# Kernel tuning notes

Measured on AMD Instinct MI355X. Metric: run time of the kernel, lower is better.

## Reference

```python
import jax, jax.numpy as jnp
import numpy as np

D_K = 64

def setup_inputs() -> dict:
    key = jax.random.key(0)
    k1, k2, k3, k4 = jax.random.split(key, 4)
    B, H, S = 2, 16, 2048
    Q = jax.random.normal(k1, (B, H, S, D_K), dtype=jnp.float32)
    K = jax.random.normal(k2, (B, H, S, D_K), dtype=jnp.float32)
    V = jax.random.normal(k3, (B, H, S, D_K), dtype=jnp.float32)
    attn_mask = jax.random.randint(k4, (B, H, S, S), 0, 2) == 1
    return {"Q": Q, "K": K, "V": V, "attn_mask": attn_mask}

def reference(Q, K, V, attn_mask):
    scale = 1.0 / np.sqrt(D_K).astype(np.float32)
    # scores: [B, H, S, S]
    scores = jnp.einsum('bhqd,bhkd->bhqk', Q, K) * scale
    scores = jnp.where(attn_mask, jnp.float32(-1e6), scores)
    scores = jax.nn.softmax(scores, axis=-1)
    context = jnp.einsum('bhqk,bhkd->bhqd', scores, V)
    return (context, scores)
```

## Files before the change

kernel.cpp:

```cpp
#include <hip/hip_runtime.h>

#define S_LEN 2048
#define NBH   32

typedef __attribute__((ext_vector_type(8))) __bf16 bf16x8;
typedef __attribute__((ext_vector_type(4))) float  f32x4;

__global__ __launch_bounds__(256) void prep_k(const float* __restrict__ K,
                                              __bf16* __restrict__ kh,
                                              __bf16* __restrict__ kl) {
    const int total = NBH * S_LEN * 64;
    for (int idx = blockIdx.x * 256 + threadIdx.x; idx < total;
         idx += gridDim.x * 256) {
        int d   = idx & 63;
        int key = (idx >> 6) & (S_LEN - 1);
        int bh  = idx >> 17;
        float f = K[idx];
        __bf16 h  = (__bf16)f;
        __bf16 lo = (__bf16)(f - (float)h);
        int dc = d >> 5, g = (d >> 3) & 3, j = d & 7;
        size_t off = ((size_t)((bh * 2 + dc) * S_LEN + key) << 5) + g * 8 + j;
        kh[off] = h;
        kl[off] = lo;
    }
}

__global__ __launch_bounds__(256) void prep_v(const float* __restrict__ V,
                                              __bf16* __restrict__ vb) {
    const int total = NBH * S_LEN * 64;
    for (int idx = blockIdx.x * 256 + threadIdx.x; idx < total;
         idx += gridDim.x * 256) {
        int n  = idx & 63;
        int k  = (idx >> 6) & (S_LEN - 1);
        int bh = idx >> 17;
        float f = V[idx];
        int kc = k >> 5, g = (k >> 3) & 3, j = k & 7;
        size_t off = ((size_t)((bh * 64 + n) * 64 + kc) << 5) + g * 8 + j;
        vb[off] = (__bf16)f;
    }
}

__global__ __launch_bounds__(512, 4) void attn_kernel(
    const float* __restrict__ Q, const int* __restrict__ mask,
    const __bf16* __restrict__ kh, const __bf16* __restrict__ kl,
    const __bf16* __restrict__ vb,
    float* __restrict__ ctxOut, float* __restrict__ scoresOut)
{
    extern __shared__ float lds[];
    __bf16* eb   = (__bf16*)lds;
    __bf16* qf   = (__bf16*)(lds + 16384);
    float*  pmax = lds + 17408;
    float*  psum = lds + 17536;
    float*  mrow = lds + 17664;
    float*  rinv = lds + 17680;
    float*  parts= lds + 17696;

    const int t   = threadIdx.x;
    const int w   = t >> 6;
    const int l   = t & 63;
    const int l15 = l & 15;
    const int lg  = l >> 4;
    const int bh  = blockIdx.y;
    const int q0  = blockIdx.x << 4;

    {
        const float* Qg = Q + ((size_t)bh * S_LEN + q0) * 64;
        #pragma unroll
        for (int e = t; e < 16 * 64; e += 512) {
            int row = e >> 6, d = e & 63;
            float fs = Qg[e] * 0.125f;
            __bf16 h  = (__bf16)fs;
            __bf16 lo = (__bf16)(fs - (float)h);
            int dc = d >> 5, g = (d >> 3) & 3, j = d & 7;
            int lane2 = (g << 4) | row;
            qf[((0 + dc) * 64 + lane2) * 8 + j] = h;
            qf[((2 + dc) * 64 + lane2) * 8 + j] = lo;
        }
    }
    __syncthreads();

    f32x4 acc[16];
    {
        bf16x8 ah0 = *(bf16x8*)&qf[(0 * 64 + l) * 8];
        bf16x8 ah1 = *(bf16x8*)&qf[(1 * 64 + l) * 8];
        bf16x8 al0 = *(bf16x8*)&qf[(2 * 64 + l) * 8];
        bf16x8 al1 = *(bf16x8*)&qf[(3 * 64 + l) * 8];

        #pragma unroll
        for (int i = 0; i < 16; ++i) {
            int kt = w + (i << 3);
            int k0 = kt << 4;
            f32x4 a = {0.f, 0.f, 0.f, 0.f};
            size_t off0 = ((size_t)((bh * 2 + 0) * S_LEN + k0 + l15) << 5) + lg * 8;
            size_t off1 = ((size_t)((bh * 2 + 1) * S_LEN + k0 + l15) << 5) + lg * 8;
            bf16x8 kh0 = *(const bf16x8*)(kh + off0);
            bf16x8 kl0 = *(const bf16x8*)(kl + off0);
            bf16x8 kh1 = *(const bf16x8*)(kh + off1);
            bf16x8 kl1 = *(const bf16x8*)(kl + off1);
            a = __builtin_amdgcn_mfma_f32_16x16x32_bf16(ah0, kh0, a, 0, 0, 0);
            a = __builtin_amdgcn_mfma_f32_16x16x32_bf16(al0, kh0, a, 0, 0, 0);
            a = __builtin_amdgcn_mfma_f32_16x16x32_bf16(ah0, kl0, a, 0, 0, 0);
            a = __builtin_amdgcn_mfma_f32_16x16x32_bf16(ah1, kh1, a, 0, 0, 0);
            a = __builtin_amdgcn_mfma_f32_16x16x32_bf16(al1, kh1, a, 0, 0, 0);
            a = __builtin_amdgcn_mfma_f32_16x16x32_bf16(ah1, kl1, a, 0, 0, 0);
            acc[i] = a;
        }
    }

    {
        f32x4 mx = acc[0];
        #pragma unroll
        for (int i = 1; i < 16; ++i) {
            mx[0] = fmaxf(mx[0], acc[i][0]);
            mx[1] = fmaxf(mx[1], acc[i][1]);
            mx[2] = fmaxf(mx[2], acc[i][2]);
            mx[3] = fmaxf(mx[3], acc[i][3]);
        }
        #pragma unroll
        for (int r = 0; r < 4; ++r) {
            float v = mx[r];
            v = fmaxf(v, __shfl_xor(v, 1, 64));
            v = fmaxf(v, __shfl_xor(v, 2, 64));
            v = fmaxf(v, __shfl_xor(v, 4, 64));
            v = fmaxf(v, __shfl_xor(v, 8, 64));
            if (l15 == 0) pmax[(w << 4) + (lg << 2) + r] = v;
        }
    }
    __syncthreads();
    if (t < 16) {
        float m = pmax[t];
        for (int ww = 1; ww < 8; ++ww) m = fmaxf(m, pmax[(ww << 4) + t]);
        mrow[t] = m;
    }
    __syncthreads();

    {
        float mr0 = mrow[(lg << 2) + 0];
        float mr1 = mrow[(lg << 2) + 1];
        float mr2 = mrow[(lg << 2) + 2];
        float mr3 = mrow[(lg << 2) + 3];
        const int* mb = mask + (size_t)bh * S_LEN * S_LEN
                             + (size_t)(q0 + (lg << 2)) * S_LEN + l15;
        f32x4 sum = {0.f, 0.f, 0.f, 0.f};
        #pragma unroll
        for (int i = 0; i < 16; ++i) {
            int kt = w + (i << 3);
            int k0 = kt << 4;
            int gc = ((kt & 1) << 1) | (l15 >> 3);
            int ebase = ((kt >> 1) << 9) | (gc << 7) | ((lg ^ gc) << 3) | (l15 & 7);
            int m0 = mb[(size_t)0 * S_LEN + k0];
            int m1 = mb[(size_t)1 * S_LEN + k0];
            int m2 = mb[(size_t)2 * S_LEN + k0];
            int m3 = mb[(size_t)3 * S_LEN + k0];
            float e0 = m0 ? 0.f : __expf(acc[i][0] - mr0);
            float e1 = m1 ? 0.f : __expf(acc[i][1] - mr1);
            float e2 = m2 ? 0.f : __expf(acc[i][2] - mr2);
            float e3 = m3 ? 0.f : __expf(acc[i][3] - mr3);
            acc[i][0] = e0; acc[i][1] = e1; acc[i][2] = e2; acc[i][3] = e3;
            sum[0] += e0; sum[1] += e1; sum[2] += e2; sum[3] += e3;
            eb[ebase +  0] = (__bf16)e0;
            eb[ebase + 32] = (__bf16)e1;
            eb[ebase + 64] = (__bf16)e2;
            eb[ebase + 96] = (__bf16)e3;
        }
        #pragma unroll
        for (int r = 0; r < 4; ++r) {
            float v = sum[r];
            v += __shfl_xor(v, 1, 64);
            v += __shfl_xor(v, 2, 64);
            v += __shfl_xor(v, 4, 64);
            v += __shfl_xor(v, 8, 64);
            if (l15 == 0) psum[(w << 4) + (lg << 2) + r] = v;
        }
    }
    __syncthreads();
    if (t < 16) {
        float s = 0.f;
        for (int ww = 0; ww < 8; ++ww) s += psum[(ww << 4) + t];
        rinv[t] = 1.0f / s;
    }
    __syncthreads();

    {
        float rv0 = rinv[(lg << 2) + 0];
        float rv1 = rinv[(lg << 2) + 1];
        float rv2 = rinv[(lg << 2) + 2];
        float rv3 = rinv[(lg << 2) + 3];
        float* sb = scoresOut + (size_t)bh * S_LEN * S_LEN
                              + (size_t)(q0 + (lg << 2)) * S_LEN + l15;
        #pragma unroll
        for (int i = 0; i < 16; ++i) {
            int k0 = (w + (i << 3)) << 4;
            sb[(size_t)0 * S_LEN + k0] = acc[i][0] * rv0;
            sb[(size_t)1 * S_LEN + k0] = acc[i][1] * rv1;
            sb[(size_t)2 * S_LEN + k0] = acc[i][2] * rv2;
            sb[(size_t)3 * S_LEN + k0] = acc[i][3] * rv3;
        }
    }

    {
        int n0    = (w & 3) << 4;
        int khalf = w >> 2;
        const int alane  = (lg << 4) | ((l15 & 3) << 2) | (l15 >> 2);
        const int alane2 = alane ^ lg;
        f32x4 o = {0.f, 0.f, 0.f, 0.f};
        const __bf16* vbase = vb + ((size_t)(bh * 64 + n0 + l15) << 11) + lg * 8;
        #pragma unroll
        for (int cc = 0; cc < 32; ++cc) {
            int c = (khalf << 5) + cc;
            bf16x8 pa = *(bf16x8*)&eb[(c << 9) + (alane2 << 3)];
            bf16x8 bv = *(const bf16x8*)(vbase + ((size_t)c << 5));
            o = __builtin_amdgcn_mfma_f32_16x16x32_bf16(pa, bv, o, 0, 0, 0);
        }
        int pbase = (w << 8) + (lg << 6) + l15;
        parts[pbase +  0] = o[0];
        parts[pbase + 16] = o[1];
        parts[pbase + 32] = o[2];
        parts[pbase + 48] = o[3];
    }
    __syncthreads();

    {
        float* cbase = ctxOut + ((size_t)bh * S_LEN + q0) * 64;
        #pragma unroll
        for (int e = t; e < 1024; e += 512) {
            int row = e >> 6, d = e & 63;
            int nt = d >> 4, ii = d & 15;
            float v = (parts[(nt << 8) + (row << 4) + ii] +
                       parts[((nt + 4) << 8) + (row << 4) + ii]) * rinv[row];
            cbase[e] = v;
        }
    }
}

extern "C" void kernel_launch(void* const* d_in, const int* in_sizes, int n_in,
                              void* d_out, int out_size, void* d_ws, size_t ws_size,
                              hipStream_t stream) {
    const float* Q    = (const float*)d_in[0];
    const float* K    = (const float*)d_in[1];
    const float* V    = (const float*)d_in[2];
    const int*   mask = (const int*)d_in[3];

    float* ctxOut    = (float*)d_out;
    float* scoresOut = ctxOut + (size_t)NBH * S_LEN * 64;

    __bf16* kh = (__bf16*)d_ws;
    __bf16* kl = kh + (size_t)NBH * S_LEN * 64;
    __bf16* vb = kl + (size_t)NBH * S_LEN * 64;

    prep_k<<<4096, 256, 0, stream>>>(K, kh, kl);
    prep_v<<<4096, 256, 0, stream>>>(V, vb);

    const int lds_bytes = 19744 * 4;
    hipFuncSetAttribute((const void*)attn_kernel,
                        hipFuncAttributeMaxDynamicSharedMemorySize, lds_bytes);

    dim3 grid(S_LEN / 16, NBH);
    attn_kernel<<<grid, 512, lds_bytes, stream>>>(Q, mask, kh, kl, vb,
                                                  ctxOut, scoresOut);
}
```

Measured before the change: 1.170 ms.

## Pre-pack boolean mask into bitwords and stage them through LDS

Adds a prep kernel that compresses the int32 attention mask into 32-bit bitmasks using vectorized int4 loads. The attention kernel loads its block's bitmask rows once at the start, parks them in LDS (reusing the Q staging area after an extra barrier), and tests bits during the exp pass. This replaces many scattered dependent global int loads in the softmax loop with a streaming pass and cheap LDS reads. The cost is an extra kernel launch and a full mask read-plus-write pass before the main kernel.

```diff
diff --git a/kernel.cpp b/kernel.cpp
--- a/kernel.cpp
+++ b/kernel.cpp
@@ -40,8 +40,27 @@
     }
 }
 
+__global__ __launch_bounds__(256) void prep_mask(const int* __restrict__ mask,
+                                                 unsigned int* __restrict__ pm) {
+    const int nwords = NBH * S_LEN * 64;
+    for (int wi = blockIdx.x * 256 + threadIdx.x; wi < nwords;
+         wi += gridDim.x * 256) {
+        const int* mp = mask + ((size_t)wi << 5);
+        unsigned int bits = 0;
+        #pragma unroll
+        for (int j = 0; j < 8; ++j) {
+            int4 m = *(const int4*)(mp + j * 4);
+            bits |= (m.x != 0 ? 1u : 0u) << (j * 4 + 0);
+            bits |= (m.y != 0 ? 1u : 0u) << (j * 4 + 1);
+            bits |= (m.z != 0 ? 1u : 0u) << (j * 4 + 2);
+            bits |= (m.w != 0 ? 1u : 0u) << (j * 4 + 3);
+        }
+        pm[wi] = bits;
+    }
+}
+
 __global__ __launch_bounds__(512, 4) void attn_kernel(
-    const float* __restrict__ Q, const int* __restrict__ mask,
+    const float* __restrict__ Q, const unsigned int* __restrict__ pm,
     const __bf16* __restrict__ kh, const __bf16* __restrict__ kl,
     const __bf16* __restrict__ vb,
     float* __restrict__ ctxOut, float* __restrict__ scoresOut)
@@ -49,6 +68,7 @@
     extern __shared__ float lds[];
     __bf16* eb   = (__bf16*)lds;
     __bf16* qf   = (__bf16*)(lds + 16384);
+    unsigned int* mlds = (unsigned int*)(lds + 16384);
     float*  pmax = lds + 17408;
     float*  psum = lds + 17536;
     float*  mrow = lds + 17664;
@@ -62,6 +82,8 @@
     const int lg  = l >> 4;
     const int bh  = blockIdx.y;
     const int q0  = blockIdx.x << 4;
+
+    uint2 mws = *(const uint2*)(pm + (((size_t)(bh * S_LEN + q0)) << 6) + (t << 1));
 
     {
         const float* Qg = Q + ((size_t)bh * S_LEN + q0) * 64;
@@ -79,13 +101,16 @@
     }
     __syncthreads();
 
+    bf16x8 ah0 = *(bf16x8*)&qf[(0 * 64 + l) * 8];
+    bf16x8 ah1 = *(bf16x8*)&qf[(1 * 64 + l) * 8];
+    bf16x8 al0 = *(bf16x8*)&qf[(2 * 64 + l) * 8];
+    bf16x8 al1 = *(bf16x8*)&qf[(3 * 64 + l) * 8];
+    __syncthreads();
+
+    *(uint2*)&mlds[t << 1] = mws;
+
     f32x4 acc[16];
     {
-        bf16x8 ah0 = *(bf16x8*)&qf[(0 * 64 + l) * 8];
-        bf16x8 ah1 = *(bf16x8*)&qf[(1 * 64 + l) * 8];
-        bf16x8 al0 = *(bf16x8*)&qf[(2 * 64 + l) * 8];
-        bf16x8 al1 = *(bf16x8*)&qf[(3 * 64 + l) * 8];
-
         #pragma unroll
         for (int i = 0; i < 16; ++i) {
             int kt = w + (i << 3);
@@ -139,23 +164,22 @@
         float mr1 = mrow[(lg << 2) + 1];
         float mr2 = mrow[(lg << 2) + 2];
         float mr3 = mrow[(lg << 2) + 3];
-        const int* mb = mask + (size_t)bh * S_LEN * S_LEN
-                             + (size_t)(q0 + (lg << 2)) * S_LEN + l15;
+        const unsigned int bp = ((w & 1) << 4) | l15;
         f32x4 sum = {0.f, 0.f, 0.f, 0.f};
         #pragma unroll
         for (int i = 0; i < 16; ++i) {
             int kt = w + (i << 3);
-            int k0 = kt << 4;
             int gc = ((kt & 1) << 1) | (l15 >> 3);
             int ebase = ((kt >> 1) << 9) | (gc << 7) | ((lg ^ gc) << 3) | (l15 & 7);
-            int m0 = mb[(size_t)0 * S_LEN + k0];
-            int m1 = mb[(size_t)1 * S_LEN + k0];
-            int m2 = mb[(size_t)2 * S_LEN + k0];
-            int m3 = mb[(size_t)3 * S_LEN + k0];
-            float e0 = m0 ? 0.f : __expf(acc[i][0] - mr0);
-            float e1 = m1 ? 0.f : __expf(acc[i][1] - mr1);
-            float e2 = m2 ? 0.f : __expf(acc[i][2] - mr2);
-            float e3 = m3 ? 0.f : __expf(acc[i][3] - mr3);
+            int wb = (i << 2) + (w >> 1);
+            unsigned int w0 = mlds[(((lg << 2) + 0) << 6) + wb];
+            unsigned int w1 = mlds[(((lg << 2) + 1) << 6) + wb];
+            unsigned int w2 = mlds[(((lg << 2) + 2) << 6) + wb];
+            unsigned int w3 = mlds[(((lg << 2) + 3) << 6) + wb];
+            float e0 = ((w0 >> bp) & 1u) ? 0.f : __expf(acc[i][0] - mr0);
+            float e1 = ((w1 >> bp) & 1u) ? 0.f : __expf(acc[i][1] - mr1);
+            float e2 = ((w2 >> bp) & 1u) ? 0.f : __expf(acc[i][2] - mr2);
+            float e3 = ((w3 >> bp) & 1u) ? 0.f : __expf(acc[i][3] - mr3);
             acc[i][0] = e0; acc[i][1] = e1; acc[i][2] = e2; acc[i][3] = e3;
             sum[0] += e0; sum[1] += e1; sum[2] += e2; sum[3] += e3;
             eb[ebase +  0] = (__bf16)e0;
@@ -244,18 +268,21 @@
     float* ctxOut    = (float*)d_out;
     float* scoresOut = ctxOut + (size_t)NBH * S_LEN * 64;
 
+    const size_t NE = (size_t)NBH * S_LEN * 64;
     __bf16* kh = (__bf16*)d_ws;
-    __bf16* kl = kh + (size_t)NBH * S_LEN * 64;
-    __bf16* vb = kl + (size_t)NBH * S_LEN * 64;
+    __bf16* kl = kh + NE;
+    __bf16* vb = kl + NE;
+    unsigned int* pmw = (unsigned int*)(vb + NE);
 
     prep_k<<<4096, 256, 0, stream>>>(K, kh, kl);
     prep_v<<<4096, 256, 0, stream>>>(V, vb);
+    prep_mask<<<4096, 256, 0, stream>>>(mask, pmw);
 
     const int lds_bytes = 19744 * 4;
     hipFuncSetAttribute((const void*)attn_kernel,
                         hipFuncAttributeMaxDynamicSharedMemorySize, lds_bytes);
 
     dim3 grid(S_LEN / 16, NBH);
-    attn_kernel<<<grid, 512, lds_bytes, stream>>>(Q, mask, kh, kl, vb,
+    attn_kernel<<<grid, 512, lds_bytes, stream>>>(Q, pmw, kh, kl, vb,
                                                   ctxOut, scoresOut);
 }
```

Result: slower. 1.302 ms (+11.3%).
